# Optimization experiments

Measured on AMD Instinct MI355X. Metric: run time of the kernel, lower is better.

Reference implementation:

```python
import jax, jax.numpy as jnp
import numpy as np
from jax import lax

DIM = 64
HEADS = 8

def conv1x1(x, w):
    # x: [B,C,H,W], w: [O,I,1,1]
    return lax.conv_general_dilated(x, w, (1, 1), 'VALID',
                                    dimension_numbers=('NCHW', 'OIHW', 'NCHW'))

def dwconv3x3(x, w):
    # depthwise 3x3, w: [C,1,3,3]
    C = x.shape[1]
    return lax.conv_general_dilated(x, w, (1, 1), ((1, 1), (1, 1)),
                                    dimension_numbers=('NCHW', 'OIHW', 'NCHW'),
                                    feature_group_count=C)

def setup_inputs() -> dict:
    key = jax.random.key(0)
    ks = jax.random.split(key, 7)
    B, C, H, W = 8, DIM, 256, 256
    x = jax.random.normal(ks[0], (B, C, H, W), dtype=jnp.float32)
    w_gate = jax.random.normal(ks[1], (C, C, 1, 1), dtype=jnp.float32) * 0.05
    w_gate_dw = jax.random.normal(ks[2], (C, 1, 3, 3), dtype=jnp.float32) * 0.05
    w_qkv = jax.random.normal(ks[3], (3 * C, C, 1, 1), dtype=jnp.float32) * 0.05
    w_qkv_dw = jax.random.normal(ks[4], (3 * C, 1, 3, 3), dtype=jnp.float32) * 0.05
    w_proj = jax.random.normal(ks[5], (C, C, 1, 1), dtype=jnp.float32) * 0.05
    temperature = jnp.ones((HEADS, 1, 1), dtype=jnp.float32)
    return {'x': x, 'w_gate': w_gate, 'w_gate_dw': w_gate_dw,
            'w_qkv': w_qkv, 'w_qkv_dw': w_qkv_dw, 'w_proj': w_proj,
            'temperature': temperature}

def reference(x, w_gate, w_gate_dw, w_qkv, w_qkv_dw, w_proj, temperature):
    b, c, h, w = x.shape
    head = HEADS
    cph = c // head  # channels per head

    gate = dwconv3x3(conv1x1(x, w_gate), w_gate_dw)  # [b,c,h,w]
    qkv = dwconv3x3(conv1x1(x, w_qkv), w_qkv_dw)     # [b,3c,h,w]
    q, k, v = jnp.split(qkv, 3, axis=1)

    def to_heads(t):
        return t.reshape(b, head, cph, h * w)  # [b,head,c',hw]
    q, k, v = to_heads(q), to_heads(k), to_heads(v)

    # L2-normalize along the spatial (hw) axis (torch F.normalize, eps=1e-12)
    q = q / jnp.maximum(jnp.linalg.norm(q, axis=-1, keepdims=True), 1e-12)
    k = k / jnp.maximum(jnp.linalg.norm(k, axis=-1, keepdims=True), 1e-12)

    # transposed attention over channels: [b,head,c',c']
    attn = jnp.einsum('bhcn,bhdn->bhcd', q, k) * temperature
    attn = jax.nn.softmax(attn, axis=-1)
    out = jnp.einsum('bhcd,bhdn->bhcn', attn, v)  # [b,head,c',hw]
    out = out.reshape(b, c, h, w)

    out = jax.nn.gelu(gate, approximate=False) * out
    out = conv1x1(out, w_proj)
    return out
```

## Files before the change

kernel.cpp:

```cpp
#include <hip/hip_runtime.h>

typedef _Float16 f16;
using f16x4 = __attribute__((ext_vector_type(4))) _Float16;
using f16x8 = __attribute__((ext_vector_type(8))) _Float16;
using f32x4 = __attribute__((ext_vector_type(4))) float;

#define HW 65536
#define NBAND 16
#define ROWS 16
#define RS 320

static __device__ __forceinline__ float my_erf(float v) {
  float x = fabsf(v);
  float t = 1.f / (1.f + 0.3275911f * x);
  float y = t * (0.254829592f + t * (-0.284496736f + t * (1.421413741f
          + t * (-1.453152027f + t * 1.061405429f))));
  float r = 1.f - y * __expf(-x * x);
  return v < 0.f ? -r : r;
}
static __device__ __forceinline__ float my_gelu(float s) {
  return 0.5f * s * (1.f + my_erf(s * 0.70710678118654752f));
}

__global__ void TRA_Attention_15281493639325_kernel() {}

__global__ void k_signal(float* out, long long n, float val) {
  long long i = (long long)blockIdx.x * blockDim.x + threadIdx.x;
  long long stride = (long long)gridDim.x * blockDim.x;
  for (; i < n; i += stride) out[i] = val;
}

__global__ __launch_bounds__(256) void k0_wconv(
    const float* __restrict__ w_gate, const float* __restrict__ w_qkv,
    f16* __restrict__ W16)
{
  int i = blockIdx.x * 256 + threadIdx.x;
  int m = i >> 4, kc = i & 15;
  const float* src = (m < 64) ? (w_gate + m*64 + kc*4)
                              : (w_qkv + (m-64)*64 + kc*4);
  float4 f = *(const float4*)src;
  f16x4 pk = { (f16)f.x, (f16)f.y, (f16)f.z, (f16)f.w };
  *(f16x4*)(W16 + m*64 + kc*4) = pk;
}

__global__ __launch_bounds__(256) void k1_mfma(
    const float* __restrict__ x, const f16* __restrict__ W16,
    f16* __restrict__ A)
{
  __shared__ __align__(16) unsigned char lds[32768];
  unsigned char* xs = lds;
  f16* os = (f16*)lds;

  const int tid = threadIdx.x, blk = blockIdx.x;
  const int b = blk >> 10;
  const long long p0 = (long long)(blk & 1023) * 64;

  for (int cid = tid; cid < 1024; cid += 256) {
    int k = cid >> 4, c = cid & 15;
    float4 f = *(const float4*)(x + ((long long)b*64 + k)*HW + p0 + c*4);
    const float* e = (const float*)&f;
    #pragma unroll
    for (int i = 0; i < 4; ++i) {
      int p = c*4 + i;
      int hp = ((p & 7) ^ ((p >> 3) & 7)) << 4;
      *(f16*)(xs + p*128 + ((2*k) ^ hp)) = (f16)e[i];
    }
  }
  __syncthreads();

  const int wave = tid >> 6, lane = tid & 63;
  const int m0 = (wave >> 1) * 128, n0 = (wave & 1) * 32;
  const int lr = lane & 15, lg = lane >> 4;

  f32x4 acc[8][2];
  #pragma unroll
  for (int i = 0; i < 8; ++i)
    #pragma unroll
    for (int j = 0; j < 2; ++j) acc[i][j] = (f32x4){0.f,0.f,0.f,0.f};

  #pragma unroll
  for (int ks = 0; ks < 2; ++ks) {
    f16x8 af[8], bfr[2];
    #pragma unroll
    for (int mi = 0; mi < 8; ++mi) {
      int m = m0 + mi*16 + lr;
      af[mi] = *(const f16x8*)(W16 + m*64 + ks*32 + lg*8);
    }
    #pragma unroll
    for (int ni = 0; ni < 2; ++ni) {
      int p = n0 + ni*16 + lr;
      int hp = ((p & 7) ^ ((p >> 3) & 7)) << 4;
      bfr[ni] = *(const f16x8*)(xs + p*128 + ((ks*64 + lg*16) ^ hp));
    }
    #pragma unroll
    for (int mi = 0; mi < 8; ++mi)
      #pragma unroll
      for (int ni = 0; ni < 2; ++ni)
        acc[mi][ni] = __builtin_amdgcn_mfma_f32_16x16x32_f16(
            af[mi], bfr[ni], acc[mi][ni], 0, 0, 0);
  }

  __syncthreads();
  #pragma unroll
  for (int mi = 0; mi < 8; ++mi)
    #pragma unroll
    for (int ni = 0; ni < 2; ++ni)
      #pragma unroll
      for (int r = 0; r < 4; ++r) {
        int m = m0 + mi*16 + lg*4 + r;
        int p = n0 + ni*16 + lr;
        os[m*64 + (p ^ ((m & 7) << 3))] = (f16)acc[mi][ni][r];
      }
  __syncthreads();

  #pragma unroll
  for (int pass = 0; pass < 8; ++pass) {
    int idx = pass*256 + tid;
    int row = idx >> 3, c8 = idx & 7;
    f16x8 v = *(const f16x8*)(lds + row*128 + ((c8 ^ (row & 7)) * 16));
    *(f16x8*)(A + ((long long)b*256 + row)*HW + p0 + c8*8) = v;
  }
}

__global__ __launch_bounds__(256) void k2a_dw(
    const f16* __restrict__ A, const float* __restrict__ w_gate_dw,
    const float* __restrict__ w_qkv_dw, f16* __restrict__ Vv, f16* __restrict__ GG)
{
  const int tid = threadIdx.x, blk = blockIdx.x;
  const int yband = blk & 3, ch2 = (blk >> 2) & 127, b = blk >> 9;
  const bool isv = ch2 >= 64;
  const int c = isv ? ch2 - 64 : ch2;
  const f16* src = A + ((long long)b*256 + (isv ? 192 + c : c)) * HW;
  const float* wsrc = isv ? (w_qkv_dw + (128 + c)*9) : (w_gate_dw + c*9);
  f16* dst = (isv ? Vv : GG) + ((long long)b*64 + c) * HW;

  float wd[9];
  #pragma unroll
  for (int j = 0; j < 9; ++j) wd[j] = wsrc[j];

  const int xc = tid & 31, ysub = tid >> 5;
  const int lane = tid & 63;
  const int xbase = xc * 8;
  const int y0 = yband * 64 + ysub * 8;

  float rb[3][10];

  auto load_row = [&](int y, float* r) {
    if (y >= 0 && y < 256) {
      uint4 raw = *(const uint4*)(src + y*256 + xbase);
      const f16* e = (const f16*)&raw;
      #pragma unroll
      for (int t = 0; t < 8; ++t) r[1 + t] = (float)e[t];
    } else {
      #pragma unroll
      for (int t = 0; t < 8; ++t) r[1 + t] = 0.f;
    }
    float lf = __shfl(r[8], lane - 1);
    float rf = __shfl(r[1], lane + 1);
    r[0] = (xc == 0)  ? 0.f : lf;
    r[9] = (xc == 31) ? 0.f : rf;
  };

  load_row(y0 - 1, rb[0]);
  load_row(y0,     rb[1]);

  #pragma unroll
  for (int i = 0; i < 8; ++i) {
    load_row(y0 + i + 1, rb[(i + 2) % 3]);
    const float* rm = rb[i % 3];
    const float* r0 = rb[(i + 1) % 3];
    const float* rp = rb[(i + 2) % 3];
    f16x8 st;
    #pragma unroll
    for (int j = 0; j < 8; ++j) {
      float s = wd[0]*rm[j] + wd[1]*rm[j+1] + wd[2]*rm[j+2]
              + wd[3]*r0[j] + wd[4]*r0[j+1] + wd[5]*r0[j+2]
              + wd[6]*rp[j] + wd[7]*rp[j+1] + wd[8]*rp[j+2];
      if (!isv) s = my_gelu(s);
      st[j] = (f16)s;
    }
    *(f16x8*)(dst + (y0 + i)*256 + xbase) = st;
  }
}

__device__ __forceinline__ int ridx(int c, int slot, int i) {
  return ((((c << 2) | slot) * RS) + i) ^ ((c & 7) << 3);
}

__global__ __launch_bounds__(64) void k2b_qk(
    const f16* __restrict__ A, const float* __restrict__ w_qkv_dw,
    float* __restrict__ GRP)
{
  __shared__ __align__(16) f16 ring[16*4*RS];
  const int lane = threadIdx.x, blk = blockIdx.x;
  const int band = blk & (NBAND-1), h = (blk >> 4) & 7, b = blk >> 7;

  const int c  = lane & 15, g  = lane >> 4;
  const int cs = lane >> 2, q4 = lane & 3;

  const int wrow = (c < 8) ? (h*8 + c) : (64 + h*8 + (c - 8));
  float wq[9];
  #pragma unroll
  for (int j = 0; j < 9; ++j) wq[j] = w_qkv_dw[wrow*9 + j];

  const f16* sbase = A + ((long long)b*256 +
      (cs < 8 ? 64 + h*8 + cs : 128 + h*8 + (cs - 8))) * HW;

  ring[ridx(cs, q4, 7)]   = (f16)0.f;
  ring[ridx(cs, q4, 264)] = (f16)0.f;

  auto load_row = [&](int yy, uint4* r) {
    if (yy >= 0 && yy < 256) {
      const f16* p = sbase + yy*256 + q4*64;
      #pragma unroll
      for (int t = 0; t < 8; ++t) r[t] = *(const uint4*)(p + t*8);
    } else {
      #pragma unroll
      for (int t = 0; t < 8; ++t) r[t] = make_uint4(0u,0u,0u,0u);
    }
  };
  auto write_row = [&](int slot, const uint4* r) {
    #pragma unroll
    for (int t = 0; t < 8; ++t)
      *(uint4*)&ring[ridx(cs, slot, 8 + q4*64 + t*8)] = r[t];
  };

  const int y0 = band * ROWS;
  {
    uint4 r[8];
    load_row(y0-1, r); write_row((y0+3)&3, r);
    load_row(y0,   r); write_row((y0+4)&3, r);
    load_row(y0+1, r); write_row((y0+5)&3, r);
  }
  __syncthreads();

  f32x4 acc = (f32x4){0.f, 0.f, 0.f, 0.f};

  for (int y = y0; y < y0 + ROWS; ++y) {
    uint4 r[8];
    const bool pf = (y + 2 <= y0 + ROWS);
    if (pf) load_row(y + 2, r);

    const int s0 = (y+3)&3, s1 = (y+4)&3, s2 = (y+5)&3;
    #pragma unroll
    for (int q = 0; q < 8; ++q) {
      const int base = 7 + q*32 + g*8;
      float v0[10], v1[10], v2[10];
      #pragma unroll
      for (int t = 0; t < 10; ++t) {
        v0[t] = (float)ring[ridx(c, s0, base+t)];
        v1[t] = (float)ring[ridx(c, s1, base+t)];
        v2[t] = (float)ring[ridx(c, s2, base+t)];
      }
      f16x8 frag;
      #pragma unroll
      for (int j = 0; j < 8; ++j) {
        float s = wq[0]*v0[j] + wq[1]*v0[j+1] + wq[2]*v0[j+2]
                + wq[3]*v1[j] + wq[4]*v1[j+1] + wq[5]*v1[j+2]
                + wq[6]*v2[j] + wq[7]*v2[j+1] + wq[8]*v2[j+2];
        frag[j] = (f16)s;
      }
      acc = __builtin_amdgcn_mfma_f32_16x16x32_f16(frag, frag, acc, 0, 0, 0);
    }
    if (pf) write_row((y+6)&3, r);
    __syncthreads();
  }

  const long long gbase = (long long)((b*8 + h)*NBAND + band) * 80;
  #pragma unroll
  for (int reg = 0; reg < 4; ++reg) {
    int rrow = g*4 + reg;
    float val = acc[reg];
    if (rrow == c) GRP[gbase + c] = val;
    else if (rrow < 8 && c >= 8) GRP[gbase + 16 + rrow*8 + (c-8)] = val;
  }
}

__global__ __launch_bounds__(64) void k2c_attn(
    const float* __restrict__ GRP, const float* __restrict__ temp,
    float* __restrict__ ATT)
{
  __shared__ float s[80];
  const int tid = threadIdx.x;
  const int h = blockIdx.x & 7, b = blockIdx.x >> 3;
  for (int i = tid; i < 80; i += 64) {
    float v = 0.f;
    for (int band = 0; band < NBAND; ++band)
      v += GRP[(((b*8 + h)*NBAND + band) * 80) + i];
    s[i] = v;
  }
  __syncthreads();
  const int c = tid >> 3, d = tid & 7;
  float nq = fmaxf(sqrtf(s[c]), 1e-12f);
  float nk = fmaxf(sqrtf(s[8 + d]), 1e-12f);
  float logit = s[16 + c*8 + d] / (nq * nk) * temp[h];
  float m = logit;
  #pragma unroll
  for (int off = 4; off; off >>= 1) m = fmaxf(m, __shfl_xor(m, off));
  float e = __expf(logit - m);
  float sum = e;
  #pragma unroll
  for (int off = 4; off; off >>= 1) sum += __shfl_xor(sum, off);
  ATT[((b*8 + h)*8 + c)*8 + d] = e / sum;
}

__global__ __launch_bounds__(256) void k3_out(
    const f16* __restrict__ Vv, const f16* __restrict__ GG,
    const float* __restrict__ ATT, const float* __restrict__ w_proj,
    float* __restrict__ out)
{
  __shared__ __align__(16) unsigned char lds[64*128 + 256*128 + 2048];
  unsigned char* wl = lds;
  unsigned char* xs = lds + 64*128;
  float* attn_s = (float*)(lds + 64*128 + 256*128);

  const int tid = threadIdx.x;
  const int y = blockIdx.x & 255, b = blockIdx.x >> 8;

  for (int cid = tid; cid < 1024; cid += 256) {
    int m = cid >> 4, kc = cid & 15;
    float4 f = *(const float4*)(w_proj + m*64 + kc*4);
    int hm = ((m & 7) ^ ((m >> 3) & 7)) << 4;
    f16x4 pk = { (f16)f.x, (f16)f.y, (f16)f.z, (f16)f.w };
    *(f16x4*)(wl + m*128 + ((kc*8) ^ hm)) = pk;
  }
  for (int i = tid; i < 512; i += 256) attn_s[i] = ATT[b*512 + i];
  __syncthreads();

  {
    const int pg = tid & 31, hd = tid >> 5;
    const long long base = ((long long)b*64 + hd*8)*HW + (long long)y*256 + pg*8;
    f16x8 vv[8], gg[8];
    #pragma unroll
    for (int d = 0; d < 8; ++d)
      vv[d] = *(const f16x8*)(Vv + base + (long long)d*HW);
    #pragma unroll
    for (int c = 0; c < 8; ++c)
      gg[c] = *(const f16x8*)(GG + base + (long long)c*HW);
    float a[8][8];
    #pragma unroll
    for (int c = 0; c < 8; ++c)
      #pragma unroll
      for (int d = 0; d < 8; ++d) a[c][d] = attn_s[hd*64 + c*8 + d];
    #pragma unroll
    for (int j = 0; j < 8; ++j) {
      int p = pg*8 + j;
      int hp = ((p & 7) ^ ((p >> 3) & 7)) << 4;
      f16x8 st;
      #pragma unroll
      for (int c = 0; c < 8; ++c) {
        float av = 0.f;
        #pragma unroll
        for (int d = 0; d < 8; ++d) av += a[c][d] * (float)vv[d][j];
        st[c] = (f16)((float)gg[c][j] * av);
      }
      *(f16x8*)(xs + p*128 + ((hd*16) ^ hp)) = st;
    }
  }
  __syncthreads();

  const int wave = tid >> 6, lane = tid & 63;
  const int n0 = wave * 64;
  const int lr = lane & 15, lg = lane >> 4;

  f32x4 acc[4][4];
  #pragma unroll
  for (int i = 0; i < 4; ++i)
    #pragma unroll
    for (int j = 0; j < 4; ++j) acc[i][j] = (f32x4){0.f,0.f,0.f,0.f};

  #pragma unroll
  for (int ks = 0; ks < 2; ++ks) {
    f16x8 af[4], bfr[4];
    #pragma unroll
    for (int mi = 0; mi < 4; ++mi) {
      int m = mi*16 + lr;
      int hm = ((m & 7) ^ ((m >> 3) & 7)) << 4;
      af[mi] = *(const f16x8*)(wl + m*128 + ((ks*64 + lg*16) ^ hm));
    }
    #pragma unroll
    for (int ni = 0; ni < 4; ++ni) {
      int p = n0 + ni*16 + lr;
      int hp = ((p & 7) ^ ((p >> 3) & 7)) << 4;
      bfr[ni] = *(const f16x8*)(xs + p*128 + ((ks*64 + lg*16) ^ hp));
    }
    #pragma unroll
    for (int mi = 0; mi < 4; ++mi)
      #pragma unroll
      for (int ni = 0; ni < 4; ++ni)
        acc[mi][ni] = __builtin_amdgcn_mfma_f32_16x16x32_f16(
            af[mi], bfr[ni], acc[mi][ni], 0, 0, 0);
  }

  const long long obase = (long long)b*64*HW + (long long)y*256;
  #pragma unroll
  for (int mi = 0; mi < 4; ++mi)
    #pragma unroll
    for (int ni = 0; ni < 4; ++ni)
      #pragma unroll
      for (int r = 0; r < 4; ++r) {
        int m = mi*16 + lg*4 + r;
        int p = n0 + ni*16 + lr;
        out[obase + (long long)m*HW + p] = acc[mi][ni][r];
      }
}

extern "C" void kernel_launch(void* const* d_in, const int* in_sizes, int n_in,
                              void* d_out, int out_size, void* d_ws, size_t ws_size,
                              hipStream_t stream)
{
  float* out = (float*)d_out;

  int mp[7] = {-1,-1,-1,-1,-1,-1,-1};
  bool ok = (n_in == 7);
  if (ok) {
    int n4 = 0;
    for (int i = 0; i < 7; ++i) {
      long s = in_sizes[i];
      if      (s == 33554432) mp[0] = i;
      else if (s == 576)      mp[2] = i;
      else if (s == 12288)    mp[3] = i;
      else if (s == 1728)     mp[4] = i;
      else if (s == 8)        mp[6] = i;
      else if (s == 4096)     { if (n4 == 0) mp[1] = i; else mp[5] = i; ++n4; }
    }
    ok = ok && (n4 == 2);
    for (int i = 0; i < 7; ++i) ok = ok && (mp[i] >= 0);
  }
  if (!ok) { k_signal<<<2048,256,0,stream>>>(out, (long long)out_size, 2000.0f); return; }
  if (out_size != 33554432) { k_signal<<<2048,256,0,stream>>>(out, (long long)out_size, 3000.0f); return; }

  const float* x    = (const float*)d_in[mp[0]];
  const float* wg   = (const float*)d_in[mp[1]];
  const float* wgd  = (const float*)d_in[mp[2]];
  const float* wqkv = (const float*)d_in[mp[3]];
  const float* wqd  = (const float*)d_in[mp[4]];
  const float* wpj  = (const float*)d_in[mp[5]];
  const float* tp   = (const float*)d_in[mp[6]];

  unsigned char* ws = (unsigned char*)d_ws;
  const size_t GRP_SZ   = 8UL*8*NBAND*80*4;
  const size_t FULL     = 402653184UL + GRP_SZ + 16384UL + 32768UL;
  const size_t PERB_GRP = 8UL*NBAND*80*4;
  const size_t PERB     = 50331648UL + PERB_GRP + 2048UL + 32768UL;

  if (ws != nullptr && ws_size >= FULL) {
    f16*   A    = (f16*)ws;
    f16*   Vv   = (f16*)(ws + 268435456UL);
    f16*   GG   = (f16*)(ws + 335544320UL);
    float* GRP  = (float*)(ws + 402653184UL);
    float* ATT  = (float*)(ws + 402653184UL + GRP_SZ);
    f16*   W16  = (f16*)(ws + 402653184UL + GRP_SZ + 16384UL);
    k0_wconv<<<16,   256, 0, stream>>>(wg, wqkv, W16);
    k1_mfma <<<8192, 256, 0, stream>>>(x, W16, A);
    k2a_dw  <<<4096, 256, 0, stream>>>(A, wgd, wqd, Vv, GG);
    k2b_qk  <<<8*8*NBAND, 64, 0, stream>>>(A, wqd, GRP);
    k2c_attn<<<64,   64,  0, stream>>>(GRP, tp, ATT);
    k3_out  <<<2048, 256, 0, stream>>>(Vv, GG, ATT, wpj, out);
  } else if (ws != nullptr && ws_size >= PERB) {
    f16*   A    = (f16*)ws;
    f16*   Vv   = (f16*)(ws + 33554432UL);
    f16*   GG   = (f16*)(ws + 41943040UL);
    float* GRP  = (float*)(ws + 50331648UL);
    float* ATT  = (float*)(ws + 50331648UL + PERB_GRP);
    f16*   W16  = (f16*)(ws + 50331648UL + PERB_GRP + 2048UL);
    k0_wconv<<<16, 256, 0, stream>>>(wg, wqkv, W16);
    for (int b = 0; b < 8; ++b) {
      const float* xb = x + (long long)b*64*HW;
      float* ob = out + (long long)b*64*HW;
      k1_mfma <<<1024, 256, 0, stream>>>(xb, W16, A);
      k2a_dw  <<<512,  256, 0, stream>>>(A, wgd, wqd, Vv, GG);
      k2b_qk  <<<8*NBAND, 64, 0, stream>>>(A, wqd, GRP);
      k2c_attn<<<8,    64,  0, stream>>>(GRP, tp, ATT);
      k3_out  <<<256,  256, 0, stream>>>(Vv, GG, ATT, wpj, ob);
    }
  } else {
    k_signal<<<2048,256,0,stream>>>(out, (long long)out_size, 1000.0f);
  }
}
```

Measured before the change: 337.2 us.

## Make k1 persistent over four tiles with register-prefetched next input tile

```diff
diff --git a/kernel.cpp b/kernel.cpp
--- a/kernel.cpp
+++ b/kernel.cpp
@@ -47,78 +47,99 @@
     const float* __restrict__ x, const f16* __restrict__ W16,
     f16* __restrict__ A)
 {
-  __shared__ __align__(16) unsigned char lds[32768];
-  unsigned char* xs = lds;
-  f16* os = (f16*)lds;
+  __shared__ __align__(16) unsigned char xs[8192];
+  __shared__ __align__(16) f16 os[256*64];
 
   const int tid = threadIdx.x, blk = blockIdx.x;
-  const int b = blk >> 10;
-  const long long p0 = (long long)(blk & 1023) * 64;
-
-  for (int cid = tid; cid < 1024; cid += 256) {
-    int k = cid >> 4, c = cid & 15;
-    float4 f = *(const float4*)(x + ((long long)b*64 + k)*HW + p0 + c*4);
-    const float* e = (const float*)&f;
-    #pragma unroll
-    for (int i = 0; i < 4; ++i) {
-      int p = c*4 + i;
-      int hp = ((p & 7) ^ ((p >> 3) & 7)) << 4;
-      *(f16*)(xs + p*128 + ((2*k) ^ hp)) = (f16)e[i];
-    }
-  }
-  __syncthreads();
+  const int b = blk >> 8;
+  const long long row0 = (long long)(blk & 255) * 256;
 
   const int wave = tid >> 6, lane = tid & 63;
   const int m0 = (wave >> 1) * 128, n0 = (wave & 1) * 32;
   const int lr = lane & 15, lg = lane >> 4;
 
-  f32x4 acc[8][2];
-  #pragma unroll
-  for (int i = 0; i < 8; ++i)
-    #pragma unroll
-    for (int j = 0; j < 2; ++j) acc[i][j] = (f32x4){0.f,0.f,0.f,0.f};
-
-  #pragma unroll
-  for (int ks = 0; ks < 2; ++ks) {
-    f16x8 af[8], bfr[2];
-    #pragma unroll
-    for (int mi = 0; mi < 8; ++mi) {
-      int m = m0 + mi*16 + lr;
-      af[mi] = *(const f16x8*)(W16 + m*64 + ks*32 + lg*8);
-    }
-    #pragma unroll
-    for (int ni = 0; ni < 2; ++ni) {
-      int p = n0 + ni*16 + lr;
-      int hp = ((p & 7) ^ ((p >> 3) & 7)) << 4;
-      bfr[ni] = *(const f16x8*)(xs + p*128 + ((ks*64 + lg*16) ^ hp));
-    }
+  float4 pre[4];
+  #pragma unroll
+  for (int i = 0; i < 4; ++i) {
+    int cid = tid + (i << 8), k = cid >> 4, c = cid & 15;
+    pre[i] = *(const float4*)(x + ((long long)b*64 + k)*HW + row0 + c*4);
+  }
+
+  for (int t = 0; t < 4; ++t) {
+    const long long p0 = row0 + t*64;
+
+    #pragma unroll
+    for (int i = 0; i < 4; ++i) {
+      int cid = tid + (i << 8), k = cid >> 4, c = cid & 15;
+      const float* e = (const float*)&pre[i];
+      #pragma unroll
+      for (int j = 0; j < 4; ++j) {
+        int p = c*4 + j;
+        int hp = ((p & 7) ^ ((p >> 3) & 7)) << 4;
+        *(f16*)(xs + p*128 + ((2*k) ^ hp)) = (f16)e[j];
+      }
+    }
+    __syncthreads();
+
+    if (t < 3) {
+      const long long pn = row0 + (t+1)*64;
+      #pragma unroll
+      for (int i = 0; i < 4; ++i) {
+        int cid = tid + (i << 8), k = cid >> 4, c = cid & 15;
+        pre[i] = *(const float4*)(x + ((long long)b*64 + k)*HW + pn + c*4);
+      }
+    }
+
+    f32x4 acc[8][2];
+    #pragma unroll
+    for (int i = 0; i < 8; ++i)
+      #pragma unroll
+      for (int j = 0; j < 2; ++j) acc[i][j] = (f32x4){0.f,0.f,0.f,0.f};
+
+    #pragma unroll
+    for (int ks = 0; ks < 2; ++ks) {
+      f16x8 af[8], bfr[2];
+      #pragma unroll
+      for (int mi = 0; mi < 8; ++mi) {
+        int m = m0 + mi*16 + lr;
+        af[mi] = *(const f16x8*)(W16 + m*64 + ks*32 + lg*8);
+      }
+      #pragma unroll
+      for (int ni = 0; ni < 2; ++ni) {
+        int p = n0 + ni*16 + lr;
+        int hp = ((p & 7) ^ ((p >> 3) & 7)) << 4;
+        bfr[ni] = *(const f16x8*)(xs + p*128 + ((ks*64 + lg*16) ^ hp));
+      }
+      #pragma unroll
+      for (int mi = 0; mi < 8; ++mi)
+        #pragma unroll
+        for (int ni = 0; ni < 2; ++ni)
+          acc[mi][ni] = __builtin_amdgcn_mfma_f32_16x16x32_f16(
+              af[mi], bfr[ni], acc[mi][ni], 0, 0, 0);
+    }
+    __syncthreads();
+
     #pragma unroll
     for (int mi = 0; mi < 8; ++mi)
       #pragma unroll
       for (int ni = 0; ni < 2; ++ni)
-        acc[mi][ni] = __builtin_amdgcn_mfma_f32_16x16x32_f16(
-            af[mi], bfr[ni], acc[mi][ni], 0, 0, 0);
-  }
-
-  __syncthreads();
-  #pragma unroll
-  for (int mi = 0; mi < 8; ++mi)
-    #pragma unroll
-    for (int ni = 0; ni < 2; ++ni)
-      #pragma unroll
-      for (int r = 0; r < 4; ++r) {
-        int m = m0 + mi*16 + lg*4 + r;
-        int p = n0 + ni*16 + lr;
-        os[m*64 + (p ^ ((m & 7) << 3))] = (f16)acc[mi][ni][r];
-      }
-  __syncthreads();
-
-  #pragma unroll
-  for (int pass = 0; pass < 8; ++pass) {
-    int idx = pass*256 + tid;
-    int row = idx >> 3, c8 = idx & 7;
-    f16x8 v = *(const f16x8*)(lds + row*128 + ((c8 ^ (row & 7)) * 16));
-    *(f16x8*)(A + ((long long)b*256 + row)*HW + p0 + c8*8) = v;
+        #pragma unroll
+        for (int r = 0; r < 4; ++r) {
+          int m = m0 + mi*16 + lg*4 + r;
+          int p = n0 + ni*16 + lr;
+          os[m*64 + (p ^ ((m & 7) << 3))] = (f16)acc[mi][ni][r];
+        }
+    __syncthreads();
+
+    #pragma unroll
+    for (int pass = 0; pass < 8; ++pass) {
+      int idx = pass*256 + tid;
+      int row = idx >> 3, c8 = idx & 7;
+      f16x8 v = *(const f16x8*)((const unsigned char*)os + row*128
+                                + ((c8 ^ (row & 7)) * 16));
+      *(f16x8*)(A + ((long long)b*256 + row)*HW + p0 + c8*8) = v;
+    }
+    __syncthreads();
   }
 }
 
@@ -452,7 +473,7 @@
     float* ATT  = (float*)(ws + 402653184UL + GRP_SZ);
     f16*   W16  = (f16*)(ws + 402653184UL + GRP_SZ + 16384UL);
     k0_wconv<<<16,   256, 0, stream>>>(wg, wqkv, W16);
-    k1_mfma <<<8192, 256, 0, stream>>>(x, W16, A);
+    k1_mfma <<<2048, 256, 0, stream>>>(x, W16, A);
     k2a_dw  <<<4096, 256, 0, stream>>>(A, wgd, wqd, Vv, GG);
     k2b_qk  <<<8*8*NBAND, 64, 0, stream>>>(A, wqd, GRP);
     k2c_attn<<<64,   64,  0, stream>>>(GRP, tp, ATT);
@@ -468,7 +489,7 @@
     for (int b = 0; b < 8; ++b) {
       const float* xb = x + (long long)b*64*HW;
       float* ob = out + (long long)b*64*HW;
-      k1_mfma <<<1024, 256, 0, stream>>>(xb, W16, A);
+      k1_mfma <<<256,  256, 0, stream>>>(xb, W16, A);
       k2a_dw  <<<512,  256, 0, stream>>>(A, wgd, wqd, Vv, GG);
       k2b_qk  <<<8*NBAND, 64, 0, stream>>>(A, wqd, GRP);
       k2c_attn<<<8,    64,  0, stream>>>(GRP, tp, ATT);
```

After: 287.7 us. -14.7%, faster.
